# Optimization experiments

Measured on AMD Instinct MI355X. Metric: run time of the kernel, lower is better.

Reference implementation:

```python
import math
import jax, jax.numpy as jnp
import numpy as np


def setup_inputs() -> dict:
    key = jax.random.key(0)
    ks = jax.random.split(key, 11)
    B, L, D = 16, 2048, 1024
    s = 0.02  # weight init scale
    return {
        "queries": jax.random.normal(ks[0], (B, L, D), jnp.float32),
        "keys": jax.random.normal(ks[1], (B, L, D), jnp.float32),
        "values": jax.random.normal(ks[2], (B, L, D), jnp.float32),
        "Wq": jax.random.normal(ks[3], (D, D), jnp.float32) * s,
        "bq": jax.random.normal(ks[4], (D,), jnp.float32) * s,
        "Wk": jax.random.normal(ks[5], (D, D), jnp.float32) * s,
        "bk": jax.random.normal(ks[6], (D,), jnp.float32) * s,
        "Wv": jax.random.normal(ks[7], (D, D), jnp.float32) * s,
        "bv": jax.random.normal(ks[8], (D,), jnp.float32) * s,
        "Wo": jax.random.normal(ks[9], (D, D), jnp.float32) * s,
        "bo": jax.random.normal(ks[10], (D,), jnp.float32) * s,
        "n_heads": 8,
    }


def reference(queries, keys, values, Wq, bq, Wk, bk, Wv, bv, Wo, bo, n_heads):
    B, L, D = queries.shape
    H = n_heads
    E = D // H
    # projections -> (B, H, E, L)
    q = (queries @ Wq.T + bq).reshape(B, L, H, E).transpose(0, 2, 3, 1)
    k = (keys @ Wk.T + bk).reshape(B, L, H, E).transpose(0, 2, 3, 1)
    v = (values @ Wv.T + bv).reshape(B, L, H, E).transpose(0, 2, 3, 1)

    # period-based dependency discovery via FFT cross-correlation
    q_fft = jnp.fft.rfft(q, axis=-1)
    k_fft = jnp.fft.rfft(k, axis=-1)
    corr = jnp.fft.irfft(q_fft * jnp.conj(k_fft), n=L, axis=-1)  # (B,H,E,L)

    # time-delay aggregation (training variant: batch-shared top-k delays)
    top_k = int(1 * math.log(L))  # factor = 1
    mean_value = corr.mean(axis=(1, 2))  # (B, L)
    _, index = jax.lax.top_k(mean_value.mean(axis=0), top_k)  # (top_k,)
    weights = mean_value[:, index]  # (B, top_k)
    tmp_corr = jax.nn.softmax(weights, axis=-1)  # (B, top_k)

    pos = jnp.arange(L)
    agg = jnp.zeros_like(v)
    for i in range(top_k):  # small fixed loop (top_k = 7)
        rolled = jnp.take(v, (pos + index[i]) % L, axis=-1)  # roll(v, -index[i])
        agg = agg + rolled * tmp_corr[:, i][:, None, None, None]

    out = agg.transpose(0, 3, 1, 2).reshape(B, L, D)  # (B,L,H,E) -> (B,L,D)
    return out @ Wo.T + bo
```

## Files before the change

kernel.cpp:

```cpp
#include <hip/hip_runtime.h>

typedef __attribute__((ext_vector_type(8))) short bf16x8;
typedef __attribute__((ext_vector_type(4))) short s16x4;
typedef __attribute__((ext_vector_type(4))) float f32x4;

__device__ __forceinline__ float bf2f(unsigned short u) {
    union { unsigned int u; float f; } x; x.u = ((unsigned int)u) << 16; return x.f;
}
__device__ __forceinline__ unsigned short f2bf(float f) {
    union { float f; unsigned int u; } x; x.f = f;
    unsigned int u = x.u;
    unsigned int r = (u + 0x7fffu + ((u >> 16) & 1u)) >> 16;
    return (unsigned short)r;
}

#define GLDS16(gp, lp)                                                        \
    __builtin_amdgcn_global_load_lds(                                         \
        (const __attribute__((address_space(1))) void*)(gp),                  \
        (__attribute__((address_space(3))) void*)(lp), 16, 0, 0)

template<int OUT_MODE>
__global__ __launch_bounds__(512, 2)
void gemm256(const unsigned short* __restrict__ A, const unsigned short* __restrict__ Bw,
             const float* __restrict__ bias, void* __restrict__ out_) {
    __shared__ __align__(16) unsigned short sA[2][16384];
    __shared__ __align__(16) unsigned short sB[2][16384];

    const int tid  = threadIdx.x;
    const int lane = tid & 63;
    const int w    = tid >> 6;
    const int wr   = w >> 2, wc = w & 3;
    const int fr   = lane & 15, g4 = lane >> 4;

    const int bid = blockIdx.x;
    const int qq  = (int)gridDim.x >> 3;
    const int swz = qq ? (bid & 7) * qq + (bid >> 3) : bid;
    const int  col0 = (swz & 3) * 256;
    const long row0 = (long)(swz >> 2) * 256;

    const int srow = tid >> 3;
    const int sj   = (tid & 7) ^ (srow & 7);
    const unsigned short* gA = A  + (size_t)(row0 + srow) * 1024 + sj * 8;
    const unsigned short* gB = Bw + (size_t)(col0 + srow) * 1024 + sj * 8;
    const int ldst = w * 1024;

    auto stage = [&](int buf, int t) {
        const unsigned short* a = gA + t * 64;
        const unsigned short* b = gB + t * 64;
        char* dA = (char*)&sA[buf][0];
        char* dB = (char*)&sB[buf][0];
#pragma unroll
        for (int r = 0; r < 4; ++r)
            GLDS16(a + r * 65536, (__attribute__((address_space(3))) char*)(dA + r * 8192 + ldst));
#pragma unroll
        for (int r = 0; r < 4; ++r)
            GLDS16(b + r * 65536, (__attribute__((address_space(3))) char*)(dB + r * 8192 + ldst));
    };

    f32x4 acc[8][4];
#pragma unroll
    for (int m = 0; m < 8; ++m)
#pragma unroll
        for (int n = 0; n < 4; ++n) acc[m][n] = (f32x4){0.f, 0.f, 0.f, 0.f};

    stage(0, 0);
    stage(1, 1);

    const int mskK = (fr & 7) << 4;

    for (int t = 0; t < 16; ++t) {
        if (t < 15) asm volatile("s_waitcnt vmcnt(8)" ::: "memory");
        else        asm volatile("s_waitcnt vmcnt(0)" ::: "memory");
        asm volatile("s_barrier" ::: "memory");
        __builtin_amdgcn_sched_barrier(0);

        const char* la = (const char*)&sA[t & 1][0];
        const char* lb = (const char*)&sB[t & 1][0];

        bf16x8 bF[2][4];
#pragma unroll
        for (int c = 0; c < 2; ++c)
#pragma unroll
            for (int n = 0; n < 4; ++n) {
                const int row = wc * 64 + n * 16 + fr;
                bF[c][n] = *(const bf16x8*)(lb + row * 128 + ((c * 64 + g4 * 16) ^ mskK));
            }
#pragma unroll
        for (int mh = 0; mh < 2; ++mh) {
            bf16x8 aF[2][4];
#pragma unroll
            for (int c = 0; c < 2; ++c)
#pragma unroll
                for (int m = 0; m < 4; ++m) {
                    const int row = wr * 128 + mh * 64 + m * 16 + fr;
                    aF[c][m] = *(const bf16x8*)(la + row * 128 + ((c * 64 + g4 * 16) ^ mskK));
                }
            __builtin_amdgcn_s_setprio(1);
#pragma unroll
            for (int c = 0; c < 2; ++c)
#pragma unroll
                for (int n = 0; n < 4; ++n)
#pragma unroll
                    for (int m = 0; m < 4; ++m)
                        acc[mh * 4 + m][n] =
                            __builtin_amdgcn_mfma_f32_16x16x32_bf16(aF[c][m], bF[c][n], acc[mh * 4 + m][n], 0, 0, 0);
            __builtin_amdgcn_s_setprio(0);
        }

        __builtin_amdgcn_sched_barrier(0);
        asm volatile("s_barrier" ::: "memory");
        if (t + 2 < 16) stage(t & 1, t + 2);
    }

    const int cr = g4 * 4;
    const int cc = fr;
    if constexpr (OUT_MODE == 2) {
        const int b  = (int)(row0 >> 11);
        const int tb = ((int)row0 & 2047) + wr * 128 + cr;
#pragma unroll
        for (int m = 0; m < 8; ++m) {
#pragma unroll
            for (int n = 0; n < 4; ++n) {
                int col = col0 + wc * 64 + n * 16 + cc;
                float bv = bias[col];
                s16x4 o;
#pragma unroll
                for (int j = 0; j < 4; ++j) o[j] = (short)f2bf(acc[m][n][j] + bv);
                *(s16x4*)&((unsigned short*)out_)[((size_t)b * 1024 + col) * 2048 + tb + m * 16] = o;
            }
        }
    } else {
#pragma unroll
        for (int m = 0; m < 8; ++m) {
            long row = row0 + wr * 128 + m * 16 + cr;
#pragma unroll
            for (int n = 0; n < 4; ++n) {
                int col = col0 + wc * 64 + n * 16 + cc;
                float bv = bias[col];
#pragma unroll
                for (int j = 0; j < 4; ++j) {
                    float v = acc[m][n][j] + bv;
                    if constexpr (OUT_MODE == 1) ((float*)out_)[(row + j) * 1024 + col] = v;
                    else ((unsigned short*)out_)[(row + j) * 1024 + col] = f2bf(v);
                }
            }
        }
    }
}

__global__ __launch_bounds__(256)
void cast_f2b(const float* __restrict__ src, unsigned short* __restrict__ dst) {
    const size_t i = ((size_t)blockIdx.x * 256 + threadIdx.x) * 8;
    f32x4 v0 = *(const f32x4*)(src + i);
    f32x4 v1 = *(const f32x4*)(src + i + 4);
    bf16x8 o;
#pragma unroll
    for (int j = 0; j < 4; ++j) o[j] = (short)f2bf(v0[j]);
#pragma unroll
    for (int j = 0; j < 4; ++j) o[4 + j] = (short)f2bf(v1[j]);
    *(bf16x8*)(dst + i) = o;
}

__global__ __launch_bounds__(256)
void cast_wT(const float* __restrict__ src, unsigned short* __restrict__ dst) {
    __shared__ float t[64][65];
    const int bx = blockIdx.x * 64, by = blockIdx.y * 64;
    const int tx = threadIdx.x & 63, ty = threadIdx.x >> 6;
    for (int r = ty; r < 64; r += 4)
        t[r][tx] = src[(size_t)(by + r) * 1024 + bx + tx];
    __syncthreads();
    for (int r = ty; r < 64; r += 4)
        dst[(size_t)(bx + r) * 1024 + by + tx] = f2bf(t[tx][r]);
}

__global__ __launch_bounds__(256)
void bias2_kernel(const float* __restrict__ Wo, const float* __restrict__ bv,
                  const float* __restrict__ bo, float* __restrict__ b2) {
    const int n = blockIdx.x * 4 + (threadIdx.x >> 6);
    const int lane = threadIdx.x & 63;
    float s = 0.f;
    for (int k = lane; k < 1024; k += 64) s += Wo[(size_t)n * 1024 + k] * bv[k];
#pragma unroll
    for (int off = 32; off > 0; off >>= 1) s += __shfl_xor(s, off, 64);
    if (lane == 0) b2[n] = s + bo[n];
}

__device__ __forceinline__ void dft8(float* xr, float* xi) {
    const float c8 = 0.70710678118654752440f;
    float es0r = xr[0] + xr[4], es0i = xi[0] + xi[4];
    float es1r = xr[0] - xr[4], es1i = xi[0] - xi[4];
    float es2r = xr[2] + xr[6], es2i = xi[2] + xi[6];
    float es3r = xr[2] - xr[6], es3i = xi[2] - xi[6];
    float E0r = es0r + es2r, E0i = es0i + es2i;
    float E2r = es0r - es2r, E2i = es0i - es2i;
    float E1r = es1r + es3i, E1i = es1i - es3r;
    float E3r = es1r - es3i, E3i = es1i + es3r;
    float os0r = xr[1] + xr[5], os0i = xi[1] + xi[5];
    float os1r = xr[1] - xr[5], os1i = xi[1] - xi[5];
    float os2r = xr[3] + xr[7], os2i = xi[3] + xi[7];
    float os3r = xr[3] - xr[7], os3i = xi[3] - xi[7];
    float O0r = os0r + os2r, O0i = os0i + os2i;
    float O2r = os0r - os2r, O2i = os0i - os2i;
    float O1r = os1r + os3i, O1i = os1i - os3r;
    float O3r = os1r - os3i, O3i = os1i + os3r;
    float p1 = c8 * (O1r + O1i), q1 = c8 * (O1i - O1r);
    float p3 = c8 * (O3r + O3i), q3 = c8 * (O3i - O3r);
    xr[0] = E0r + O0r; xi[0] = E0i + O0i;
    xr[4] = E0r - O0r; xi[4] = E0i - O0i;
    xr[1] = E1r + p1;  xi[1] = E1i + q1;
    xr[5] = E1r - p1;  xi[5] = E1i - q1;
    xr[2] = E2r + O2i; xi[2] = E2i - O2r;
    xr[6] = E2r - O2i; xi[6] = E2i + O2r;
    xr[3] = E3r + q3;  xi[3] = E3i - p3;
    xr[7] = E3r - q3;  xi[7] = E3i + p3;
}

__device__ __forceinline__ int ps(int p) { return p ^ (((p >> 5) & 7) << 2); }

#define TWIDDLE2(wr_, wi_)                                                    \
    {                                                                         \
        float cr_ = (wr_), ci_ = (wi_);                                       \
        _Pragma("unroll")                                                     \
        for (int k = 1; k < 8; ++k) {                                         \
            float t0 = ar[k] * cr_ - ai[k] * ci_;                             \
            float t1 = ar[k] * ci_ + ai[k] * cr_;                             \
            ar[k] = t0; ai[k] = t1;                                           \
            float t2 = br[k] * cr_ - bi[k] * ci_;                             \
            float t3 = br[k] * ci_ + bi[k] * cr_;                             \
            br[k] = t2; bi[k] = t3;                                           \
            if (k < 7) {                                                      \
                float nr = cr_ * (wr_) - ci_ * (wi_);                         \
                float ni = cr_ * (wi_) + ci_ * (wr_);                         \
                cr_ = nr; ci_ = ni;                                           \
            }                                                                 \
        }                                                                     \
    }

__global__ __launch_bounds__(256)
void fft_corr(const float* __restrict__ qf, const unsigned short* __restrict__ kt,
              float* __restrict__ G) {
    __shared__ float2 za[2048];
    __shared__ float2 zb[2048];
    const int tid = threadIdx.x;
    const int bid = blockIdx.x;
    const int swzb = (bid & 7) * 256 + (bid >> 3);
    const int b = swzb >> 7;
    const int chunk = swzb & 127;

    const float N2PI = -6.28318530717958647692f;
    float w1r, w1i, w2r, w2i, w3r, w3i;
    {
        float s, c;
        __sincosf(N2PI * (float)tid * (1.0f / 2048.0f), &s, &c); w1r = c; w1i = s;
        __sincosf(N2PI * (float)(tid & 31) * (1.0f / 256.0f), &s, &c); w2r = c; w2i = s;
        __sincosf(N2PI * (float)(tid & 3) * (1.0f / 32.0f),  &s, &c); w3r = c; w3i = s;
    }

    float aR0 = 0.f, aI0 = 0.f, aR1 = 0.f, aI1 = 0.f;
    float aR2 = 0.f, aI2 = 0.f, aR3 = 0.f, aI3 = 0.f, aR4 = 0.f;

    const int beta = tid >> 5, s2 = tid & 31;
    const int gam  = tid >> 2, u3 = tid & 3;

    for (int it = 0; it < 4; ++it) {
        const int d0 = chunk * 8 + it * 2;
        const float* qbase = qf + (size_t)b * 2048 * 1024 + d0;
        const unsigned short* k0 = kt + ((size_t)b * 1024 + d0) * 2048;
        const unsigned short* k1 = k0 + 2048;

        float ar[8], ai[8], br[8], bi[8];
#pragma unroll
        for (int k = 0; k < 8; ++k) {
            const int t = tid + 256 * k;
            float2 qv = *(const float2*)(qbase + (size_t)t * 1024);
            ar[k] = qv.x; br[k] = qv.y;
            ai[k] = bf2f(k0[t]); bi[k] = bf2f(k1[t]);
        }
        dft8(ar, ai); dft8(br, bi);
        TWIDDLE2(w1r, w1i)
#pragma unroll
        for (int k = 0; k < 8; ++k) {
            const int p = ps(256 * k + tid);
            za[p] = make_float2(ar[k], ai[k]);
            zb[p] = make_float2(br[k], bi[k]);
        }
        __syncthreads();

#pragma unroll
        for (int k = 0; k < 8; ++k) {
            const int p = ps(256 * beta + 32 * k + s2);
            float2 va = za[p]; ar[k] = va.x; ai[k] = va.y;
            float2 vb = zb[p]; br[k] = vb.x; bi[k] = vb.y;
        }
        dft8(ar, ai); dft8(br, bi);
        TWIDDLE2(w2r, w2i)
#pragma unroll
        for (int k = 0; k < 8; ++k) {
            const int p = ps(256 * beta + 32 * k + s2);
            za[p] = make_float2(ar[k], ai[k]);
            zb[p] = make_float2(br[k], bi[k]);
        }
        __syncthreads();

#pragma unroll
        for (int k = 0; k < 8; ++k) {
            const int p = ps(32 * gam + 4 * k + u3);
            float2 va = za[p]; ar[k] = va.x; ai[k] = va.y;
            float2 vb = zb[p]; br[k] = vb.x; bi[k] = vb.y;
        }
        dft8(ar, ai); dft8(br, bi);
        TWIDDLE2(w3r, w3i)
#pragma unroll
        for (int k = 0; k < 8; ++k) {
            const int p = ps(32 * gam + 4 * k + u3);
            za[p] = make_float2(ar[k], ai[k]);
            zb[p] = make_float2(br[k], bi[k]);
        }
        __syncthreads();

#pragma unroll
        for (int k = 0; k < 8; ++k) {
            const int p = ps(8 * tid + k);
            float2 va = za[p]; ar[k] = va.x; ai[k] = va.y;
            float2 vb = zb[p]; br[k] = vb.x; bi[k] = vb.y;
        }
        __syncthreads();

#pragma unroll
        for (int blk = 0; blk < 2; ++blk) {
            const int o = 4 * blk;
            {
                float s0r = ar[o] + ar[o + 2], s0i = ai[o] + ai[o + 2];
                float s1r = ar[o] - ar[o + 2], s1i = ai[o] - ai[o + 2];
                float s2r = ar[o + 1] + ar[o + 3], s2i = ai[o + 1] + ai[o + 3];
                float s3r = ar[o + 1] - ar[o + 3], s3i = ai[o + 1] - ai[o + 3];
                ar[o + 0] = s0r + s2r; ai[o + 0] = s0i + s2i;
                ar[o + 2] = s0r - s2r; ai[o + 2] = s0i - s2i;
                ar[o + 1] = s1r + s3i; ai[o + 1] = s1i - s3r;
                ar[o + 3] = s1r - s3i; ai[o + 3] = s1i + s3r;
            }
            {
                float s0r = br[o] + br[o + 2], s0i = bi[o] + bi[o + 2];
                float s1r = br[o] - br[o + 2], s1i = bi[o] - bi[o + 2];
                float s2r = br[o + 1] + br[o + 3], s2i = bi[o + 1] + bi[o + 3];
                float s3r = br[o + 1] - br[o + 3], s3i = bi[o + 1] - bi[o + 3];
                br[o + 0] = s0r + s2r; bi[o + 0] = s0i + s2i;
                br[o + 2] = s0r - s2r; bi[o + 2] = s0i - s2i;
                br[o + 1] = s1r + s3i; bi[o + 1] = s1i - s3r;
                br[o + 3] = s1r - s3i; bi[o + 3] = s1i + s3r;
            }
        }
        {
            const int k1d = tid >> 5;
            const int k2d = (tid >> 2) & 7;
            const int fb = k1d + 8 * k2d;
#pragma unroll
            for (int blk = 0; blk < 2; ++blk) {
                const int k3d = (2 * (tid & 3) + blk) & 7;
#pragma unroll
                for (int k4 = 0; k4 < 4; ++k4) {
                    const int f = fb + 64 * k3d + 512 * k4;
                    const int pf = ps(f);
                    za[pf] = make_float2(ar[4 * blk + k4], ai[4 * blk + k4]);
                    zb[pf] = make_float2(br[4 * blk + k4], bi[4 * blk + k4]);
                }
            }
        }
        __syncthreads();

#pragma unroll
        for (int k = 0; k < 4; ++k) {
            const int f = tid + 256 * k;
            const int f2 = (2048 - f) & 2047;
            const int pf = ps(f), pf2 = ps(f2);
            float2 Za = za[pf], Ya = za[pf2];
            float Qr = 0.5f * (Za.x + Ya.x), Qi = 0.5f * (Za.y - Ya.y);
            float Kr = 0.5f * (Za.y + Ya.y), Ki = -0.5f * (Za.x - Ya.x);
            float dR = Qr * Kr + Qi * Ki;
            float dI = Qi * Kr - Qr * Ki;
            float2 Zb = zb[pf], Yb = zb[pf2];
            Qr = 0.5f * (Zb.x + Yb.x); Qi = 0.5f * (Zb.y - Yb.y);
            Kr = 0.5f * (Zb.y + Yb.y); Ki = -0.5f * (Zb.x - Yb.x);
            dR += Qr * Kr + Qi * Ki;
            dI += Qi * Kr - Qr * Ki;
            if      (k == 0) { aR0 += dR; aI0 += dI; }
            else if (k == 1) { aR1 += dR; aI1 += dI; }
            else if (k == 2) { aR2 += dR; aI2 += dI; }
            else             { aR3 += dR; aI3 += dI; }
        }
        if (tid == 0) {
            const int pf = ps(1024);
            aR4 += za[pf].x * za[pf].y + zb[pf].x * zb[pf].y;
        }
        __syncthreads();
    }

    atomicAdd(&G[((size_t)b * 1025 + tid +   0) * 2 + 0], aR0);
    atomicAdd(&G[((size_t)b * 1025 + tid +   0) * 2 + 1], aI0);
    atomicAdd(&G[((size_t)b * 1025 + tid + 256) * 2 + 0], aR1);
    atomicAdd(&G[((size_t)b * 1025 + tid + 256) * 2 + 1], aI1);
    atomicAdd(&G[((size_t)b * 1025 + tid + 512) * 2 + 0], aR2);
    atomicAdd(&G[((size_t)b * 1025 + tid + 512) * 2 + 1], aI2);
    atomicAdd(&G[((size_t)b * 1025 + tid + 768) * 2 + 0], aR3);
    atomicAdd(&G[((size_t)b * 1025 + tid + 768) * 2 + 1], aI3);
    if (tid == 0)
        atomicAdd(&G[((size_t)b * 1025 + 1024) * 2 + 0], aR4);
}

__device__ __forceinline__ void fft2048(float* zr, float* zi,
                                        const float* twr, const float* twi, int tid) {
    for (int t = tid; t < 2048; t += 256) {
        int j = __brev((unsigned)t) >> 21;
        if (j > t) {
            float a = zr[t]; zr[t] = zr[j]; zr[j] = a;
            float c = zi[t]; zi[t] = zi[j]; zi[j] = c;
        }
    }
    __syncthreads();
    for (int s = 0; s < 11; ++s) {
        const int m = 1 << s;
        for (int i = tid; i < 1024; i += 256) {
            const int pos = i & (m - 1);
            const int i1  = ((i >> s) << (s + 1)) + pos;
            const int i2  = i1 + m;
            const int tw  = pos << (10 - s);
            float wr = twr[tw], wi = twi[tw];
            float xr = zr[i2], xi = zi[i2];
            float tr = wr * xr - wi * xi;
            float ti = wr * xi + wi * xr;
            float ur = zr[i1], ui = zi[i1];
            zr[i2] = ur - tr; zi[i2] = ui - ti;
            zr[i1] = ur + tr; zi[i1] = ui + ti;
        }
        __syncthreads();
    }
}

__device__ __forceinline__ void init_twiddle(float* twr, float* twi, int tid) {
    for (int j = tid; j < 1024; j += 256) {
        float ang = -6.28318530717958647692f * (float)j * (1.0f / 2048.0f);
        twr[j] = cosf(ang);
        twi[j] = sinf(ang);
    }
}

__global__ __launch_bounds__(256)
void irfft_mean(const float* __restrict__ G, float* __restrict__ mv) {
    __shared__ float zr[2048], zi[2048];
    __shared__ float twr[1024], twi[1024];
    const int tid = threadIdx.x;
    const int b = blockIdx.x;
    init_twiddle(twr, twi, tid);
    for (int f = tid; f < 2048; f += 256) {
        int g = (f <= 1024) ? f : 2048 - f;
        float gr = G[((size_t)b * 1025 + g) * 2 + 0];
        float gi = G[((size_t)b * 1025 + g) * 2 + 1];
        zr[f] = gr;
        zi[f] = (f <= 1024) ? -gi : gi;
    }
    __syncthreads();
    fft2048(zr, zi, twr, twi, tid);
    const float sc = 1.0f / (2048.0f * 1024.0f);
    for (int t = tid; t < 2048; t += 256) mv[b * 2048 + t] = zr[t] * sc;
}

__global__ __launch_bounds__(256)
void topk_softmax(const float* __restrict__ mv, int* __restrict__ idx_out,
                  float* __restrict__ w_out) {
    __shared__ float cm[2048];
    __shared__ float wv4[4];
    __shared__ int   wi4[4];
    __shared__ int   sel[7];
    const int tid  = threadIdx.x;
    const int lane = tid & 63;
    const int wvid = tid >> 6;

    for (int t = tid; t < 2048; t += 256) {
        float s = 0.f;
        for (int b = 0; b < 16; ++b) s += mv[b * 2048 + t];
        cm[t] = s * (1.0f / 16.0f);
    }
    __syncthreads();

    for (int it = 0; it < 7; ++it) {
        float best = -3.4e38f; int bi = 1 << 30;
#pragma unroll
        for (int q = 0; q < 8; ++q) {
            const int t = tid + q * 256;
            float v = cm[t];
            if (v > best || (v == best && t < bi)) { best = v; bi = t; }
        }
#pragma unroll
        for (int off = 32; off > 0; off >>= 1) {
            float ov = __shfl_xor(best, off, 64);
            int   oi = __shfl_xor(bi,   off, 64);
            if (ov > best || (ov == best && oi < bi)) { best = ov; bi = oi; }
        }
        if (lane == 0) { wv4[wvid] = best; wi4[wvid] = bi; }
        __syncthreads();
        if (tid == 0) {
            float bb = wv4[0]; int bj = wi4[0];
#pragma unroll
            for (int u = 1; u < 4; ++u)
                if (wv4[u] > bb || (wv4[u] == bb && wi4[u] < bj)) { bb = wv4[u]; bj = wi4[u]; }
            sel[it] = bj;
            idx_out[it] = bj;
            cm[bj] = -3.4e38f;
        }
        __syncthreads();
    }

    if (tid < 16) {
        const int b = tid;
        float wv[7]; float mx = -3.4e38f;
#pragma unroll
        for (int i = 0; i < 7; ++i) { wv[i] = mv[b * 2048 + sel[i]]; mx = fmaxf(mx, wv[i]); }
        float s = 0.f;
#pragma unroll
        for (int i = 0; i < 7; ++i) { wv[i] = expf(wv[i] - mx); s += wv[i]; }
        float inv = 1.0f / s;
#pragma unroll
        for (int i = 0; i < 7; ++i) w_out[b * 7 + i] = wv[i] * inv;
    }
}

__global__ __launch_bounds__(256)
void agg_kernel(const float* __restrict__ vsrc, const int* __restrict__ idx,
                const float* __restrict__ w, unsigned short* __restrict__ agg) {
    const int b  = blockIdx.y;
    const int t  = blockIdx.x * 2 + (threadIdx.x >> 7);
    const int d8 = (threadIdx.x & 127) * 8;
    float av[8] = {0.f, 0.f, 0.f, 0.f, 0.f, 0.f, 0.f, 0.f};
#pragma unroll
    for (int i = 0; i < 7; ++i) {
        const int srow = (t + idx[i]) & 2047;
        const float wi = w[b * 7 + i];
        const float* src = vsrc + ((size_t)b * 2048 + srow) * 1024 + d8;
        f32x4 v0 = *(const f32x4*)src;
        f32x4 v1 = *(const f32x4*)(src + 4);
#pragma unroll
        for (int j = 0; j < 4; ++j) av[j] += wi * v0[j];
#pragma unroll
        for (int j = 0; j < 4; ++j) av[4 + j] += wi * v1[j];
    }
    bf16x8 o;
#pragma unroll
    for (int j = 0; j < 8; ++j) o[j] = (short)f2bf(av[j]);
    *(bf16x8*)&agg[((size_t)b * 2048 + t) * 1024 + d8] = o;
}

__global__ __launch_bounds__(256)
void cast_w(const float* __restrict__ src, unsigned short* __restrict__ dst) {
    const int i = (blockIdx.x * 256 + threadIdx.x) * 4;
    f32x4 v = *(const f32x4*)(src + i);
    s16x4 o;
#pragma unroll
    for (int j = 0; j < 4; ++j) o[j] = (short)f2bf(v[j]);
    *(s16x4*)(dst + i) = o;
}

__global__ __launch_bounds__(256)
void zero_f32(float* __restrict__ p, int n) {
    const int i = blockIdx.x * 256 + threadIdx.x;
    if (i < n) p[i] = 0.0f;
}

extern "C" void kernel_launch(void* const* d_in, const int* in_sizes, int n_in,
                              void* d_out, int out_size, void* d_ws, size_t ws_size,
                              hipStream_t stream) {
    const float* queries = (const float*)d_in[0];
    const float* keys    = (const float*)d_in[1];
    const float* values  = (const float*)d_in[2];
    const float* Wq = (const float*)d_in[3];  const float* bq = (const float*)d_in[4];
    const float* Wk = (const float*)d_in[5];  const float* bk = (const float*)d_in[6];
    const float* Wv = (const float*)d_in[7];  const float* bv = (const float*)d_in[8];
    const float* Wo = (const float*)d_in[9];  const float* bo = (const float*)d_in[10];
    float* out = (float*)d_out;

    char* ws = (char*)d_ws;
    constexpr size_t SZP = (size_t)32768 * 1024 * 2;
    unsigned short* agg = (unsigned short*)(ws);
    unsigned short* kt  = (unsigned short*)(ws + SZP);
    unsigned short* ab  = (unsigned short*)(ws + 3 * SZP);
    unsigned short* wo  = ab;
    unsigned short* wvT = ab + 1048576;
    unsigned short* wqT = ab + 2097152;
    unsigned short* wkT = ab + 3145728;
    unsigned short* W2  = (unsigned short*)(ws + 4 * SZP);
    unsigned short* M   = W2 + 1048576;
    char* tail = ws + 4 * SZP + 4194304;
    float* zb1024 = (float*)(tail);
    float* b2     = (float*)(tail + 4096);
    float* G      = (float*)(tail + 8192);
    float* mv     = (float*)(tail + 8192 + 131328);
    int*   idx    = (int*)  (tail + 8192 + 131328 + 131072);
    float* wsm    = (float*)(tail + 8192 + 131328 + 131072 + 64);

    cast_w<<<1024, 256, 0, stream>>>(Wo, wo);
    cast_wT<<<dim3(16, 16), 256, 0, stream>>>(Wv, wvT);
    cast_wT<<<dim3(16, 16), 256, 0, stream>>>(Wq, wqT);
    cast_wT<<<dim3(16, 16), 256, 0, stream>>>(Wk, wkT);
    zero_f32<<<(32800 + 255) / 256, 256, 0, stream>>>(G, 32800);
    zero_f32<<<4, 256, 0, stream>>>(zb1024, 1024);
    bias2_kernel<<<256, 256, 0, stream>>>(Wo, bv, bo, b2);
    gemm256<0><<<16, 512, 0, stream>>>(wo, wvT, zb1024, W2);
    gemm256<0><<<16, 512, 0, stream>>>(wqT, wkT, zb1024, M);

    cast_f2b<<<16384, 256, 0, stream>>>(keys, ab);
    gemm256<2><<<512, 512, 0, stream>>>(ab, M, zb1024, kt);

    fft_corr<<<2048, 256, 0, stream>>>(queries, kt, G);
    irfft_mean<<<16, 256, 0, stream>>>(G, mv);
    topk_softmax<<<1, 256, 0, stream>>>(mv, idx, wsm);
    agg_kernel<<<dim3(1024, 16), 256, 0, stream>>>(values, idx, wsm, agg);
    gemm256<1><<<512, 512, 0, stream>>>(agg, W2, b2, out);
}
```

Baseline: 561.8 us.

## Merge weight-prep kernels, pair small GEMMs, and preload queries in fft_corr

Seven small preparation launches (weight casts and transposes, buffer zeroing, fused bias) become one block-dispatched prep_all kernel. The two 16-block weight-product GEMMs become a single 32-block gemm_pair launch, which cuts launch overhead and lets both run at once. Separately, fft_corr now loads each thread's eight query columns into registers once as float4 vectors, replacing strided float2 loads in each of four iterations. This adds register pressure in fft_corr, which could lower occupancy.

```diff
diff --git a/kernel.cpp b/kernel.cpp
--- a/kernel.cpp
+++ b/kernel.cpp
@@ -3,6 +3,7 @@
 typedef __attribute__((ext_vector_type(8))) short bf16x8;
 typedef __attribute__((ext_vector_type(4))) short s16x4;
 typedef __attribute__((ext_vector_type(4))) float f32x4;
+typedef unsigned short ushort_t;
 
 __device__ __forceinline__ float bf2f(unsigned short u) {
     union { unsigned int u; float f; } x; x.u = ((unsigned int)u) << 16; return x.f;
@@ -18,6 +19,132 @@
     __builtin_amdgcn_global_load_lds(                                         \
         (const __attribute__((address_space(1))) void*)(gp),                  \
         (__attribute__((address_space(3))) void*)(lp), 16, 0, 0)
+
+template<int OUT_MODE>
+__device__ __forceinline__
+void gemm_body(const unsigned short* __restrict__ A, const unsigned short* __restrict__ Bw,
+               const float* __restrict__ bias, void* __restrict__ out_,
+               int bid, int nb, unsigned short* sAp, unsigned short* sBp) {
+    const int tid  = threadIdx.x;
+    const int lane = tid & 63;
+    const int w    = tid >> 6;
+    const int wr   = w >> 2, wc = w & 3;
+    const int fr   = lane & 15, g4 = lane >> 4;
+
+    const int qq  = nb >> 3;
+    const int swz = qq ? (bid & 7) * qq + (bid >> 3) : bid;
+    const int  col0 = (swz & 3) * 256;
+    const long row0 = (long)(swz >> 2) * 256;
+
+    const int srow = tid >> 3;
+    const int sj   = (tid & 7) ^ (srow & 7);
+    const unsigned short* gA = A  + (size_t)(row0 + srow) * 1024 + sj * 8;
+    const unsigned short* gB = Bw + (size_t)(col0 + srow) * 1024 + sj * 8;
+    const int ldst = w * 1024;
+
+    auto stage = [&](int buf, int t) {
+        const unsigned short* a = gA + t * 64;
+        const unsigned short* b = gB + t * 64;
+        char* dA = (char*)(sAp + buf * 16384);
+        char* dB = (char*)(sBp + buf * 16384);
+#pragma unroll
+        for (int r = 0; r < 4; ++r)
+            GLDS16(a + r * 65536, (__attribute__((address_space(3))) char*)(dA + r * 8192 + ldst));
+#pragma unroll
+        for (int r = 0; r < 4; ++r)
+            GLDS16(b + r * 65536, (__attribute__((address_space(3))) char*)(dB + r * 8192 + ldst));
+    };
+
+    f32x4 acc[8][4];
+#pragma unroll
+    for (int m = 0; m < 8; ++m)
+#pragma unroll
+        for (int n = 0; n < 4; ++n) acc[m][n] = (f32x4){0.f, 0.f, 0.f, 0.f};
+
+    stage(0, 0);
+    stage(1, 1);
+
+    const int mskK = (fr & 7) << 4;
+
+    for (int t = 0; t < 16; ++t) {
+        if (t < 15) asm volatile("s_waitcnt vmcnt(8)" ::: "memory");
+        else        asm volatile("s_waitcnt vmcnt(0)" ::: "memory");
+        asm volatile("s_barrier" ::: "memory");
+        __builtin_amdgcn_sched_barrier(0);
+
+        const char* la = (const char*)(sAp + (t & 1) * 16384);
+        const char* lb = (const char*)(sBp + (t & 1) * 16384);
+
+        bf16x8 bF[2][4];
+#pragma unroll
+        for (int c = 0; c < 2; ++c)
+#pragma unroll
+            for (int n = 0; n < 4; ++n) {
+                const int row = wc * 64 + n * 16 + fr;
+                bF[c][n] = *(const bf16x8*)(lb + row * 128 + ((c * 64 + g4 * 16) ^ mskK));
+            }
+#pragma unroll
+        for (int mh = 0; mh < 2; ++mh) {
+            bf16x8 aF[2][4];
+#pragma unroll
+            for (int c = 0; c < 2; ++c)
+#pragma unroll
+                for (int m = 0; m < 4; ++m) {
+                    const int row = wr * 128 + mh * 64 + m * 16 + fr;
+                    aF[c][m] = *(const bf16x8*)(la + row * 128 + ((c * 64 + g4 * 16) ^ mskK));
+                }
+            __builtin_amdgcn_s_setprio(1);
+#pragma unroll
+            for (int c = 0; c < 2; ++c)
+#pragma unroll
+                for (int n = 0; n < 4; ++n)
+#pragma unroll
+                    for (int m = 0; m < 4; ++m)
+                        acc[mh * 4 + m][n] =
+                            __builtin_amdgcn_mfma_f32_16x16x32_bf16(aF[c][m], bF[c][n], acc[mh * 4 + m][n], 0, 0, 0);
+            __builtin_amdgcn_s_setprio(0);
+        }
+
+        __builtin_amdgcn_sched_barrier(0);
+        asm volatile("s_barrier" ::: "memory");
+        if (t + 2 < 16) stage(t & 1, t + 2);
+    }
+
+    const int cr = g4 * 4;
+    const int cc = fr;
+    if constexpr (OUT_MODE == 2) {
+        const int b  = (int)(row0 >> 11);
+        const int tb = ((int)row0 & 2047) + wr * 128 + cr;
+#pragma unroll
+        for (int m = 0; m < 8; ++m) {
+#pragma unroll
+            for (int n = 0; n < 4; ++n) {
+                int col = col0 + wc * 64 + n * 16 + cc;
+                float bv = bias[col];
+                s16x4 o;
+#pragma unroll
+                for (int j = 0; j < 4; ++j) o[j] = (short)f2bf(acc[m][n][j] + bv);
+                *(s16x4*)&((unsigned short*)out_)[((size_t)b * 1024 + col) * 2048 + tb + m * 16] = o;
+            }
+        }
+    } else {
+#pragma unroll
+        for (int m = 0; m < 8; ++m) {
+            long row = row0 + wr * 128 + m * 16 + cr;
+#pragma unroll
+            for (int n = 0; n < 4; ++n) {
+                int col = col0 + wc * 64 + n * 16 + cc;
+                float bv = bias[col];
+#pragma unroll
+                for (int j = 0; j < 4; ++j) {
+                    float v = acc[m][n][j] + bv;
+                    if constexpr (OUT_MODE == 1) ((float*)out_)[(row + j) * 1024 + col] = v;
+                    else ((unsigned short*)out_)[(row + j) * 1024 + col] = f2bf(v);
+                }
+            }
+        }
+    }
+}
 
 template<int OUT_MODE>
 __global__ __launch_bounds__(512, 2)
@@ -25,127 +152,20 @@
              const float* __restrict__ bias, void* __restrict__ out_) {
     __shared__ __align__(16) unsigned short sA[2][16384];
     __shared__ __align__(16) unsigned short sB[2][16384];
-
-    const int tid  = threadIdx.x;
-    const int lane = tid & 63;
-    const int w    = tid >> 6;
-    const int wr   = w >> 2, wc = w & 3;
-    const int fr   = lane & 15, g4 = lane >> 4;
-
-    const int bid = blockIdx.x;
-    const int qq  = (int)gridDim.x >> 3;
-    const int swz = qq ? (bid & 7) * qq + (bid >> 3) : bid;
-    const int  col0 = (swz & 3) * 256;
-    const long row0 = (long)(swz >> 2) * 256;
-
-    const int srow = tid >> 3;
-    const int sj   = (tid & 7) ^ (srow & 7);
-    const unsigned short* gA = A  + (size_t)(row0 + srow) * 1024 + sj * 8;
-    const unsigned short* gB = Bw + (size_t)(col0 + srow) * 1024 + sj * 8;
-    const int ldst = w * 1024;
-
-    auto stage = [&](int buf, int t) {
-        const unsigned short* a = gA + t * 64;
-        const unsigned short* b = gB + t * 64;
-        char* dA = (char*)&sA[buf][0];
-        char* dB = (char*)&sB[buf][0];
-#pragma unroll
-        for (int r = 0; r < 4; ++r)
-            GLDS16(a + r * 65536, (__attribute__((address_space(3))) char*)(dA + r * 8192 + ldst));
-#pragma unroll
-        for (int r = 0; r < 4; ++r)
-            GLDS16(b + r * 65536, (__attribute__((address_space(3))) char*)(dB + r * 8192 + ldst));
-    };
-
-    f32x4 acc[8][4];
-#pragma unroll
-    for (int m = 0; m < 8; ++m)
-#pragma unroll
-        for (int n = 0; n < 4; ++n) acc[m][n] = (f32x4){0.f, 0.f, 0.f, 0.f};
-
-    stage(0, 0);
-    stage(1, 1);
-
-    const int mskK = (fr & 7) << 4;
-
-    for (int t = 0; t < 16; ++t) {
-        if (t < 15) asm volatile("s_waitcnt vmcnt(8)" ::: "memory");
-        else        asm volatile("s_waitcnt vmcnt(0)" ::: "memory");
-        asm volatile("s_barrier" ::: "memory");
-        __builtin_amdgcn_sched_barrier(0);
-
-        const char* la = (const char*)&sA[t & 1][0];
-        const char* lb = (const char*)&sB[t & 1][0];
-
-        bf16x8 bF[2][4];
-#pragma unroll
-        for (int c = 0; c < 2; ++c)
-#pragma unroll
-            for (int n = 0; n < 4; ++n) {
-                const int row = wc * 64 + n * 16 + fr;
-                bF[c][n] = *(const bf16x8*)(lb + row * 128 + ((c * 64 + g4 * 16) ^ mskK));
-            }
-#pragma unroll
-        for (int mh = 0; mh < 2; ++mh) {
-            bf16x8 aF[2][4];
-#pragma unroll
-            for (int c = 0; c < 2; ++c)
-#pragma unroll
-                for (int m = 0; m < 4; ++m) {
-                    const int row = wr * 128 + mh * 64 + m * 16 + fr;
-                    aF[c][m] = *(const bf16x8*)(la + row * 128 + ((c * 64 + g4 * 16) ^ mskK));
-                }
-            __builtin_amdgcn_s_setprio(1);
-#pragma unroll
-            for (int c = 0; c < 2; ++c)
-#pragma unroll
-                for (int n = 0; n < 4; ++n)
-#pragma unroll
-                    for (int m = 0; m < 4; ++m)
-                        acc[mh * 4 + m][n] =
-                            __builtin_amdgcn_mfma_f32_16x16x32_bf16(aF[c][m], bF[c][n], acc[mh * 4 + m][n], 0, 0, 0);
-            __builtin_amdgcn_s_setprio(0);
-        }
-
-        __builtin_amdgcn_sched_barrier(0);
-        asm volatile("s_barrier" ::: "memory");
-        if (t + 2 < 16) stage(t & 1, t + 2);
-    }
-
-    const int cr = g4 * 4;
-    const int cc = fr;
-    if constexpr (OUT_MODE == 2) {
-        const int b  = (int)(row0 >> 11);
-        const int tb = ((int)row0 & 2047) + wr * 128 + cr;
-#pragma unroll
-        for (int m = 0; m < 8; ++m) {
-#pragma unroll
-            for (int n = 0; n < 4; ++n) {
-                int col = col0 + wc * 64 + n * 16 + cc;
-                float bv = bias[col];
-                s16x4 o;
-#pragma unroll
-                for (int j = 0; j < 4; ++j) o[j] = (short)f2bf(acc[m][n][j] + bv);
-                *(s16x4*)&((unsigned short*)out_)[((size_t)b * 1024 + col) * 2048 + tb + m * 16] = o;
-            }
-        }
-    } else {
-#pragma unroll
-        for (int m = 0; m < 8; ++m) {
-            long row = row0 + wr * 128 + m * 16 + cr;
-#pragma unroll
-            for (int n = 0; n < 4; ++n) {
-                int col = col0 + wc * 64 + n * 16 + cc;
-                float bv = bias[col];
-#pragma unroll
-                for (int j = 0; j < 4; ++j) {
-                    float v = acc[m][n][j] + bv;
-                    if constexpr (OUT_MODE == 1) ((float*)out_)[(row + j) * 1024 + col] = v;
-                    else ((unsigned short*)out_)[(row + j) * 1024 + col] = f2bf(v);
-                }
-            }
-        }
-    }
+    gemm_body<OUT_MODE>(A, Bw, bias, out_, blockIdx.x, gridDim.x, &sA[0][0], &sB[0][0]);
+}
+
+__global__ __launch_bounds__(512, 2)
+void gemm_pair(const unsigned short* __restrict__ A0, const unsigned short* __restrict__ B0,
+               const float* __restrict__ bias0, void* __restrict__ o0,
+               const unsigned short* __restrict__ A1, const unsigned short* __restrict__ B1,
+               const float* __restrict__ bias1, void* __restrict__ o1) {
+    __shared__ __align__(16) unsigned short sA[2][16384];
+    __shared__ __align__(16) unsigned short sB[2][16384];
+    if (blockIdx.x < 16)
+        gemm_body<0>(A0, B0, bias0, o0, blockIdx.x, 16, &sA[0][0], &sB[0][0]);
+    else
+        gemm_body<0>(A1, B1, bias1, o1, blockIdx.x - 16, 16, &sA[0][0], &sB[0][0]);
 }
 
 __global__ __launch_bounds__(256)
@@ -162,27 +182,57 @@
 }
 
 __global__ __launch_bounds__(256)
-void cast_wT(const float* __restrict__ src, unsigned short* __restrict__ dst) {
-    __shared__ float t[64][65];
-    const int bx = blockIdx.x * 64, by = blockIdx.y * 64;
-    const int tx = threadIdx.x & 63, ty = threadIdx.x >> 6;
-    for (int r = ty; r < 64; r += 4)
-        t[r][tx] = src[(size_t)(by + r) * 1024 + bx + tx];
-    __syncthreads();
-    for (int r = ty; r < 64; r += 4)
-        dst[(size_t)(bx + r) * 1024 + by + tx] = f2bf(t[tx][r]);
-}
-
-__global__ __launch_bounds__(256)
-void bias2_kernel(const float* __restrict__ Wo, const float* __restrict__ bv,
-                  const float* __restrict__ bo, float* __restrict__ b2) {
-    const int n = blockIdx.x * 4 + (threadIdx.x >> 6);
-    const int lane = threadIdx.x & 63;
-    float s = 0.f;
-    for (int k = lane; k < 1024; k += 64) s += Wo[(size_t)n * 1024 + k] * bv[k];
-#pragma unroll
-    for (int off = 32; off > 0; off >>= 1) s += __shfl_xor(s, off, 64);
-    if (lane == 0) b2[n] = s + bo[n];
+void prep_all(const float* __restrict__ Wq, const float* __restrict__ Wk,
+              const float* __restrict__ Wv, const float* __restrict__ Wo,
+              const float* __restrict__ bv, const float* __restrict__ bo,
+              unsigned short* __restrict__ wo, unsigned short* __restrict__ wvT,
+              unsigned short* __restrict__ wqT, unsigned short* __restrict__ wkT,
+              float* __restrict__ G, float* __restrict__ zb, float* __restrict__ b2) {
+    __shared__ float tsm[64][65];
+    const int bx  = blockIdx.x;
+    const int tid = threadIdx.x;
+
+    if (bx < 768) {
+        const float* src = (bx < 256) ? Wv : (bx < 512) ? Wq : Wk;
+        unsigned short* dst = (bx < 256) ? wvT : (bx < 512) ? wqT : wkT;
+        const int t  = bx & 255;
+        const int b0 = (t & 15) * 64;
+        const int by = (t >> 4) * 64;
+        const int tx = tid & 63, ty = tid >> 6;
+        for (int r = ty; r < 64; r += 4)
+            tsm[r][tx] = src[(size_t)(by + r) * 1024 + b0 + tx];
+        __syncthreads();
+        for (int r = ty; r < 64; r += 4)
+            dst[(size_t)(b0 + r) * 1024 + by + tx] = f2bf(tsm[tx][r]);
+    } else if (bx < 1024) {
+        const int base = (bx - 768) * 4096 + tid * 4;
+#pragma unroll
+        for (int r = 0; r < 4; ++r) {
+            const int i = base + r * 1024;
+            f32x4 v = *(const f32x4*)(Wo + i);
+            s16x4 o;
+#pragma unroll
+            for (int j = 0; j < 4; ++j) o[j] = (short)f2bf(v[j]);
+            *(s16x4*)(wo + i) = o;
+        }
+    } else if (bx < 1033) {
+        const int base = (bx - 1024) * 4096;
+#pragma unroll
+        for (int r = 0; r < 16; ++r) {
+            const int i = base + r * 256 + tid;
+            if (i < 32800) G[i] = 0.0f;
+        }
+    } else if (bx == 1033) {
+        *(f32x4*)(zb + tid * 4) = (f32x4){0.f, 0.f, 0.f, 0.f};
+    } else {
+        const int n = (bx - 1034) * 4 + (tid >> 6);
+        const int lane = tid & 63;
+        float s = 0.f;
+        for (int k = lane; k < 1024; k += 64) s += Wo[(size_t)n * 1024 + k] * bv[k];
+#pragma unroll
+        for (int off = 32; off > 0; off >>= 1) s += __shfl_xor(s, off, 64);
+        if (lane == 0) b2[n] = s + bo[n];
+    }
 }
 
 __device__ __forceinline__ void dft8(float* xr, float* xi) {
@@ -256,6 +306,17 @@
         __sincosf(N2PI * (float)(tid & 3) * (1.0f / 32.0f),  &s, &c); w3r = c; w3i = s;
     }
 
+    f32x4 qreg0[8], qreg1[8];
+    {
+        const float* qb0 = qf + (size_t)b * 2048 * 1024 + chunk * 8;
+#pragma unroll
+        for (int k = 0; k < 8; ++k) {
+            const float* p = qb0 + (size_t)(tid + 256 * k) * 1024;
+            qreg0[k] = *(const f32x4*)p;
+            qreg1[k] = *(const f32x4*)(p + 4);
+        }
+    }
+
     float aR0 = 0.f, aI0 = 0.f, aR1 = 0.f, aI1 = 0.f;
     float aR2 = 0.f, aI2 = 0.f, aR3 = 0.f, aI3 = 0.f, aR4 = 0.f;
 
@@ -264,7 +325,6 @@
 
     for (int it = 0; it < 4; ++it) {
         const int d0 = chunk * 8 + it * 2;
-        const float* qbase = qf + (size_t)b * 2048 * 1024 + d0;
         const unsigned short* k0 = kt + ((size_t)b * 1024 + d0) * 2048;
         const unsigned short* k1 = k0 + 2048;
 
@@ -272,8 +332,10 @@
 #pragma unroll
         for (int k = 0; k < 8; ++k) {
             const int t = tid + 256 * k;
-            float2 qv = *(const float2*)(qbase + (size_t)t * 1024);
-            ar[k] = qv.x; br[k] = qv.y;
+            f32x4 v = (it & 2) ? qreg1[k] : qreg0[k];
+            float qa = (it & 1) ? v[2] : v[0];
+            float qb = (it & 1) ? v[3] : v[1];
+            ar[k] = qa; br[k] = qb;
             ai[k] = bf2f(k0[t]); bi[k] = bf2f(k1[t]);
         }
         dft8(ar, ai); dft8(br, bi);
@@ -549,30 +611,14 @@
     *(bf16x8*)&agg[((size_t)b * 2048 + t) * 1024 + d8] = o;
 }
 
-__global__ __launch_bounds__(256)
-void cast_w(const float* __restrict__ src, unsigned short* __restrict__ dst) {
-    const int i = (blockIdx.x * 256 + threadIdx.x) * 4;
-    f32x4 v = *(const f32x4*)(src + i);
-    s16x4 o;
-#pragma unroll
-    for (int j = 0; j < 4; ++j) o[j] = (short)f2bf(v[j]);
-    *(s16x4*)(dst + i) = o;
-}
-
-__global__ __launch_bounds__(256)
-void zero_f32(float* __restrict__ p, int n) {
-    const int i = blockIdx.x * 256 + threadIdx.x;
-    if (i < n) p[i] = 0.0f;
-}
-
 extern "C" void kernel_launch(void* const* d_in, const int* in_sizes, int n_in,
                               void* d_out, int out_size, void* d_ws, size_t ws_size,
                               hipStream_t stream) {
     const float* queries = (const float*)d_in[0];
     const float* keys    = (const float*)d_in[1];
     const float* values  = (const float*)d_in[2];
-    const float* Wq = (const float*)d_in[3];  const float* bq = (const float*)d_in[4];
-    const float* Wk = (const float*)d_in[5];  const float* bk = (const float*)d_in[6];
+    const float* Wq = (const float*)d_in[3];
+    const float* Wk = (const float*)d_in[5];
     const float* Wv = (const float*)d_in[7];  const float* bv = (const float*)d_in[8];
     const float* Wo = (const float*)d_in[9];  const float* bo = (const float*)d_in[10];
     float* out = (float*)d_out;
@@ -596,16 +642,10 @@
     int*   idx    = (int*)  (tail + 8192 + 131328 + 131072);
     float* wsm    = (float*)(tail + 8192 + 131328 + 131072 + 64);
 
-    cast_w<<<1024, 256, 0, stream>>>(Wo, wo);
-    cast_wT<<<dim3(16, 16), 256, 0, stream>>>(Wv, wvT);
-    cast_wT<<<dim3(16, 16), 256, 0, stream>>>(Wq, wqT);
-    cast_wT<<<dim3(16, 16), 256, 0, stream>>>(Wk, wkT);
-    zero_f32<<<(32800 + 255) / 256, 256, 0, stream>>>(G, 32800);
-    zero_f32<<<4, 256, 0, stream>>>(zb1024, 1024);
-    bias2_kernel<<<256, 256, 0, stream>>>(Wo, bv, bo, b2);
-    gemm256<0><<<16, 512, 0, stream>>>(wo, wvT, zb1024, W2);
-    gemm256<0><<<16, 512, 0, stream>>>(wqT, wkT, zb1024, M);
-
+    prep_all<<<1290, 256, 0, stream>>>(Wq, Wk, Wv, Wo, bv, bo,
+                                       wo, wvT, wqT, wkT, G, zb1024, b2);
+    gemm_pair<<<32, 512, 0, stream>>>(wo, wvT, zb1024, W2,
+                                      wqT, wkT, zb1024, M);
     cast_f2b<<<16384, 256, 0, stream>>>(keys, ab);
     gemm256<2><<<512, 512, 0, stream>>>(ab, M, zb1024, kt);
 
```

Measured after the change: 536.8 us. -4.4%, faster.
